# Optimization experiments

Measured on AMD Instinct MI355X. Metric: run time of the kernel, lower is better.

## Reference

```python
import jax, jax.numpy as jnp
import numpy as np

N = 100000      # nodes
E = 640000      # edges
VOCAB = 100     # Embedding(num_embeddings=100)
EMB = 10        # embed_dim
H = 128         # GCN hidden width


def gcn_conv(x, W, b, src, dst, n):
    """PyG GCNConv: linear (no bias) -> add self loops -> sym-normalized scatter-add -> +bias."""
    x = x @ W                                  # [n, out]
    loop = jnp.arange(n, dtype=src.dtype)
    src2 = jnp.concatenate([src, loop])        # [E+n]
    dst2 = jnp.concatenate([dst, loop])
    deg = jax.ops.segment_sum(jnp.ones_like(dst2, dtype=x.dtype), dst2, num_segments=n)
    dinv = jnp.where(deg > 0, jax.lax.rsqrt(deg), 0.0)
    norm = dinv[src2] * dinv[dst2]             # [E+n]
    out = jax.ops.segment_sum(x[src2] * norm[:, None], dst2, num_segments=n)
    return out + b


def setup_inputs() -> dict:
    key = jax.random.key(0)
    ks = jax.random.split(key, 9)
    x = jax.random.randint(ks[0], (N, 1), 0, VOCAB, dtype=jnp.int32)
    edge_index = jax.random.randint(ks[1], (2, E), 0, N, dtype=jnp.int32)
    batch = jnp.zeros((N,), dtype=jnp.int32)
    emb = jax.random.normal(ks[2], (VOCAB, EMB), dtype=jnp.float32)
    W1 = jax.random.normal(ks[3], (EMB, H), dtype=jnp.float32) * 0.1
    b1 = jnp.zeros((H,), dtype=jnp.float32)
    W2 = jax.random.normal(ks[4], (H, H), dtype=jnp.float32) * 0.1
    b2 = jnp.zeros((H,), dtype=jnp.float32)
    W3 = jax.random.normal(ks[5], (H, 1), dtype=jnp.float32) * 0.1
    b3 = jnp.zeros((1,), dtype=jnp.float32)
    return {"x": x, "edge_index": edge_index, "batch": batch,
            "emb": emb, "W1": W1, "b1": b1, "W2": W2, "b2": b2, "W3": W3, "b3": b3}


def reference(x, edge_index, batch, emb, W1, b1, W2, b2, W3, b3):
    # eval mode: dropout(p=0.5) is identity
    h = emb[x[:, 0]]                           # [N, EMB] embedding lookup + squeeze
    src, dst = edge_index[0], edge_index[1]
    n = h.shape[0]
    h = jax.nn.relu(gcn_conv(h, W1, b1, src, dst, n))   # [N, 128]
    h = jax.nn.relu(gcn_conv(h, W2, b2, src, dst, n))   # [N, 128]
    out = jax.nn.sigmoid((h @ W3 + b3).reshape(-1))      # [N]
    return out
```

## Files before the change

kernel.cpp:

```cpp
#include <hip/hip_runtime.h>
#include <math.h>

#define HDIM 128
#define EMBD 10
#define CAP  32
#define ZSTRIDE 136

typedef __attribute__((ext_vector_type(8))) short short8;
typedef __attribute__((ext_vector_type(8))) unsigned short ushort8;
typedef __attribute__((ext_vector_type(4))) float float4a;
typedef __attribute__((ext_vector_type(2))) float float2a;
typedef __attribute__((ext_vector_type(2))) unsigned uint2a;

__device__ inline ushort bf16_rne(float f) {
    unsigned u = __float_as_uint(f);
    unsigned r = (u + 0x7fffu + ((u >> 16) & 1u)) >> 16;
    return (ushort)r;
}
__device__ inline float bf16_to_f(ushort u) {
    return __uint_as_float(((unsigned)u) << 16);
}

__global__ void k_prep(const float* __restrict__ emb, const float* __restrict__ W1,
                       const float* __restrict__ W2, ushort* __restrict__ Tb,
                       ushort* __restrict__ W2t, int* __restrict__ cnt,
                       int N, int vocab) {
    int t = blockIdx.x * 256 + threadIdx.x;
    if (t < N) cnt[t] = 0;
    if (t < vocab * HDIM) {
        int c = t >> 7, f = t & 127;
        float s = 0.f;
#pragma unroll
        for (int k = 0; k < EMBD; ++k) s += emb[c * EMBD + k] * W1[k * HDIM + f];
        Tb[t] = bf16_rne(s);
    }
    if (t < HDIM * HDIM) {
        int n = t >> 7, k = t & 127;
        W2t[t] = bf16_rne(W2[k * HDIM + n]);
    }
}

__global__ void k_fill(const int* __restrict__ src, const int* __restrict__ dst,
                       int* __restrict__ cnt, int* __restrict__ slot, int E) {
    int e = blockIdx.x * blockDim.x + threadIdx.x;
    if (e >= E) return;
    int d = dst[e];
    int p = atomicAdd(&cnt[d], 1);
    if (p < CAP) slot[(size_t)d * CAP + p] = src[e];
}

__global__ void k_meta(const int* __restrict__ x, const int* __restrict__ cnt,
                       unsigned* __restrict__ meta, int N) {
    int v = blockIdx.x * 256 + threadIdx.x;
    if (v >= N) return;
    meta[v] = ((unsigned)x[v] << 16) | (unsigned)bf16_rne(rsqrtf((float)cnt[v] + 1.0f));
}

__global__ __launch_bounds__(512) void k_gather1(const int* __restrict__ slot,
                                                 const int* __restrict__ cnt,
                                                 const unsigned* __restrict__ meta,
                                                 const ushort* __restrict__ Tb,
                                                 const float* __restrict__ b1,
                                                 unsigned char* __restrict__ Ap,
                                                 int N, int vocab) {
    __shared__ ushort TbL[100 * HDIM];
    int n8 = (vocab * HDIM) >> 3;
    for (int i = threadIdx.x; i < n8; i += 512)
        ((ushort8*)TbL)[i] = ((const ushort8*)Tb)[i];
    __syncthreads();

    int tid = blockIdx.x * 512 + threadIdx.x;
    int v = tid >> 4, q = tid & 15;
    if (v >= N) return;
    int deg = cnt[v];
    int m = min(deg, CAP);
    float dv = rsqrtf((float)deg + 1.0f);
    int total = m + 1;
    const int* slotv = slot + (size_t)v * CAP;

    float acc[8] = {0.f, 0.f, 0.f, 0.f, 0.f, 0.f, 0.f, 0.f};
    for (int base = 0; base < total; base += 8) {
        int4 sa = *(const int4*)(slotv + base);
        int4 sb = *(const int4*)(slotv + base + 4);
        int sv[8] = {sa.x, sa.y, sa.z, sa.w, sb.x, sb.y, sb.z, sb.w};
        const unsigned* mp[8];
#pragma unroll
        for (int t = 0; t < 8; ++t) {
            int idx = base + t;
            mp[t] = meta + ((idx < m) ? sv[t] : v);
        }
        unsigned m0, m1, m2, m3, m4, m5, m6, m7;
        asm volatile(
            "global_load_dword %0, %8, off\n\t"
            "global_load_dword %1, %9, off\n\t"
            "global_load_dword %2, %10, off\n\t"
            "global_load_dword %3, %11, off\n\t"
            "global_load_dword %4, %12, off\n\t"
            "global_load_dword %5, %13, off\n\t"
            "global_load_dword %6, %14, off\n\t"
            "global_load_dword %7, %15, off\n\t"
            "s_waitcnt vmcnt(0)"
            : "=&v"(m0), "=&v"(m1), "=&v"(m2), "=&v"(m3),
              "=&v"(m4), "=&v"(m5), "=&v"(m6), "=&v"(m7)
            : "v"(mp[0]), "v"(mp[1]), "v"(mp[2]), "v"(mp[3]),
              "v"(mp[4]), "v"(mp[5]), "v"(mp[6]), "v"(mp[7]));
        unsigned mm[8] = {m0, m1, m2, m3, m4, m5, m6, m7};
#pragma unroll
        for (int t = 0; t < 8; ++t) {
            float wt = (base + t <= m) ? bf16_to_f((ushort)(mm[t] & 0xffffu)) : 0.f;
            ushort8 y = *(const ushort8*)&TbL[(mm[t] >> 16) * HDIM + q * 8];
#pragma unroll
            for (int k = 0; k < 8; ++k) acc[k] += wt * bf16_to_f(y[k]);
        }
    }
    float4 bb0 = *(const float4*)(b1 + q * 8);
    float4 bb1 = *(const float4*)(b1 + q * 8 + 4);
    float bb[8] = {bb0.x, bb0.y, bb0.z, bb0.w, bb1.x, bb1.y, bb1.z, bb1.w};
    float o[8];
#pragma unroll
    for (int k = 0; k < 8; ++k)
        o[k] = dv * fmaxf(dv * acc[k] + bb[k], 0.f);
    unsigned lo = __builtin_amdgcn_cvt_pk_fp8_f32(o[0], o[1], 0u, false);
    lo = __builtin_amdgcn_cvt_pk_fp8_f32(o[2], o[3], lo, true);
    unsigned hi = __builtin_amdgcn_cvt_pk_fp8_f32(o[4], o[5], 0u, false);
    hi = __builtin_amdgcn_cvt_pk_fp8_f32(o[6], o[7], hi, true);
    uint2 ow = make_uint2(lo, hi);
    *(uint2*)(Ap + (size_t)v * HDIM + q * 8) = ow;
}

__global__ __launch_bounds__(256, 8) void k_conv2(const int* __restrict__ slot,
                                                  const int* __restrict__ cnt,
                                                  const unsigned char* __restrict__ Ap,
                                                  const ushort* __restrict__ W2t,
                                                  const float* __restrict__ b2,
                                                  const float* __restrict__ W3,
                                                  const float* __restrict__ b3,
                                                  float* __restrict__ out, int N) {
    __shared__ ushort Z[16 * ZSTRIDE];
    __shared__ float pbuf[4][16];
    int tid = threadIdx.x;
    int g = tid >> 4, q = tid & 15;
    int v0 = blockIdx.x * 16;
    int v = min(v0 + g, N - 1);

    int deg = cnt[v];
    int m = min(deg, CAP);
    float dv = rsqrtf((float)deg + 1.0f);
    int total = m + 1;
    const int* slotv = slot + (size_t)v * CAP;
    const unsigned char* aq = Ap + q * 8;

    float acc[8] = {0.f, 0.f, 0.f, 0.f, 0.f, 0.f, 0.f, 0.f};
    for (int base = 0; base < total; base += 8) {
        int4 sa = *(const int4*)(slotv + base);
        int4 sb = *(const int4*)(slotv + base + 4);
        int sv[8] = {sa.x, sa.y, sa.z, sa.w, sb.x, sb.y, sb.z, sb.w};
        const unsigned char* pp[8];
#pragma unroll
        for (int t = 0; t < 8; ++t) {
            int idx = base + t;
            int s = (idx < m) ? sv[t] : v;
            pp[t] = aq + (size_t)s * HDIM;
        }
        uint2a r0, r1, r2, r3, r4, r5, r6, r7;
        asm volatile(
            "global_load_dwordx2 %0, %8, off\n\t"
            "global_load_dwordx2 %1, %9, off\n\t"
            "global_load_dwordx2 %2, %10, off\n\t"
            "global_load_dwordx2 %3, %11, off\n\t"
            "global_load_dwordx2 %4, %12, off\n\t"
            "global_load_dwordx2 %5, %13, off\n\t"
            "global_load_dwordx2 %6, %14, off\n\t"
            "global_load_dwordx2 %7, %15, off\n\t"
            "s_waitcnt vmcnt(0)"
            : "=&v"(r0), "=&v"(r1), "=&v"(r2), "=&v"(r3),
              "=&v"(r4), "=&v"(r5), "=&v"(r6), "=&v"(r7)
            : "v"(pp[0]), "v"(pp[1]), "v"(pp[2]), "v"(pp[3]),
              "v"(pp[4]), "v"(pp[5]), "v"(pp[6]), "v"(pp[7]));
        uint2a rr[8] = {r0, r1, r2, r3, r4, r5, r6, r7};
#pragma unroll
        for (int t = 0; t < 8; ++t) {
            float wt = (base + t <= m) ? 1.f : 0.f;
            float2a f01 = __builtin_amdgcn_cvt_pk_f32_fp8(rr[t][0], false);
            float2a f23 = __builtin_amdgcn_cvt_pk_f32_fp8(rr[t][0], true);
            float2a f45 = __builtin_amdgcn_cvt_pk_f32_fp8(rr[t][1], false);
            float2a f67 = __builtin_amdgcn_cvt_pk_f32_fp8(rr[t][1], true);
            acc[0] += wt * f01.x; acc[1] += wt * f01.y;
            acc[2] += wt * f23.x; acc[3] += wt * f23.y;
            acc[4] += wt * f45.x; acc[5] += wt * f45.y;
            acc[6] += wt * f67.x; acc[7] += wt * f67.y;
        }
    }
    ushort8 z;
#pragma unroll
    for (int k = 0; k < 8; ++k) z[k] = bf16_rne(dv * acc[k]);
    *(ushort8*)&Z[g * ZSTRIDE + q * 8] = z;
    __syncthreads();

    int lane = tid & 63, w = tid >> 6;
    int l15 = lane & 15, g4 = lane >> 4;
    short8 af[4];
#pragma unroll
    for (int kt = 0; kt < 4; ++kt)
        af[kt] = *(const short8*)&Z[l15 * ZSTRIDE + kt * 32 + g4 * 8];

    float pr[4] = {0.f, 0.f, 0.f, 0.f};
#pragma unroll
    for (int i = 0; i < 2; ++i) {
        int nt = w * 2 + i;
        int col = nt * 16 + l15;
        const ushort* bp = W2t + (size_t)col * HDIM + g4 * 8;
        float4a accD = {0.f, 0.f, 0.f, 0.f};
#pragma unroll
        for (int kt = 0; kt < 4; ++kt) {
            short8 bf = *(const short8*)(bp + kt * 32);
            accD = __builtin_amdgcn_mfma_f32_16x16x32_bf16(af[kt], bf, accD, 0, 0, 0);
        }
        float bc = b2[col], wc = W3[col];
#pragma unroll
        for (int r = 0; r < 4; ++r)
            pr[r] += fmaxf(accD[r] + bc, 0.f) * wc;
    }
#pragma unroll
    for (int off = 1; off < 16; off <<= 1) {
#pragma unroll
        for (int r = 0; r < 4; ++r) pr[r] += __shfl_xor(pr[r], off, 16);
    }
    if (l15 == 0) {
#pragma unroll
        for (int r = 0; r < 4; ++r) pbuf[w][g4 * 4 + r] = pr[r];
    }
    __syncthreads();
    if (tid < 16) {
        int row = tid;
        float s = pbuf[0][row] + pbuf[1][row] + pbuf[2][row] + pbuf[3][row];
        int vr = v0 + row;
        if (vr < N) out[vr] = 1.f / (1.f + expf(-(s + b3[0])));
    }
}

extern "C" void kernel_launch(void* const* d_in, const int* in_sizes, int n_in,
                              void* d_out, int out_size, void* d_ws, size_t ws_size,
                              hipStream_t stream) {
    const int*   x    = (const int*)d_in[0];
    const int*   ei   = (const int*)d_in[1];
    const float* emb  = (const float*)d_in[3];
    const float* W1   = (const float*)d_in[4];
    const float* b1   = (const float*)d_in[5];
    const float* W2   = (const float*)d_in[6];
    const float* b2   = (const float*)d_in[7];
    const float* W3   = (const float*)d_in[8];
    const float* b3   = (const float*)d_in[9];
    float*       out  = (float*)d_out;

    int N = in_sizes[0];
    int E = in_sizes[1] / 2;
    int vocab = in_sizes[3] / EMBD;
    const int* src = ei;
    const int* dst = ei + E;

    char* w = (char*)d_ws;
    ushort*        Tb   = (ushort*)w;         w += (size_t)vocab * HDIM * 2;
    unsigned char* Ap   = (unsigned char*)w;  w += (size_t)N * HDIM;
    ushort*        W2t  = (ushort*)w;         w += (size_t)HDIM * HDIM * 2;
    int*           cnt  = (int*)w;            w += (size_t)N * 4;
    unsigned*      meta = (unsigned*)w;       w += (size_t)N * 4;
    int*           slot = (int*)w;            w += (size_t)N * CAP * 4 + 64;

    int prep_elems = N;
    if (vocab * HDIM > prep_elems) prep_elems = vocab * HDIM;
    if (HDIM * HDIM > prep_elems) prep_elems = HDIM * HDIM;
    k_prep<<<(prep_elems + 255) / 256, 256, 0, stream>>>(emb, W1, W2, Tb, W2t, cnt, N, vocab);
    k_fill<<<(E + 255) / 256, 256, 0, stream>>>(src, dst, cnt, slot, E);
    k_meta<<<(N + 255) / 256, 256, 0, stream>>>(x, cnt, meta, N);

    int g1blocks = (int)(((long long)N * 16 + 511) / 512);
    k_gather1<<<g1blocks, 512, 0, stream>>>(slot, cnt, meta, Tb, b1, Ap, N, vocab);

    int cblocks = (N + 15) / 16;
    k_conv2<<<cblocks, 256, 0, stream>>>(slot, cnt, Ap, W2t, b2, W3, b3, out, N);
}
```

Measured before the change: 178.5 us.

## Process 32 nodes per block in conv2 with 16-byte fp8 gathers

Each conv2 block now handles 32 nodes instead of 16. Each thread owns 16 features and fetches them with dwordx4 loads instead of dwordx2, which halves the gather load instructions per edge and lets each block's W2 fragment loads feed twice as many rows in the MFMA stage. Each wave now computes 4 output column tiles for one 16-row block instead of 2 tiles. Register pressure rises (16 accumulators and wider load registers), and the launch bound occupancy hint drops from 8 to 6, which risks less latency hiding on the irregular gathers.

After: 174.8 us. -2.1%, faster.

```diff
diff --git a/kernel.cpp b/kernel.cpp
--- a/kernel.cpp
+++ b/kernel.cpp
@@ -11,6 +11,7 @@
 typedef __attribute__((ext_vector_type(4))) float float4a;
 typedef __attribute__((ext_vector_type(2))) float float2a;
 typedef __attribute__((ext_vector_type(2))) unsigned uint2a;
+typedef __attribute__((ext_vector_type(4))) unsigned uint4a;
 
 __device__ inline ushort bf16_rne(float f) {
     unsigned u = __float_as_uint(f);
@@ -128,7 +129,7 @@
     *(uint2*)(Ap + (size_t)v * HDIM + q * 8) = ow;
 }
 
-__global__ __launch_bounds__(256, 8) void k_conv2(const int* __restrict__ slot,
+__global__ __launch_bounds__(256, 6) void k_conv2(const int* __restrict__ slot,
                                                   const int* __restrict__ cnt,
                                                   const unsigned char* __restrict__ Ap,
                                                   const ushort* __restrict__ W2t,
@@ -136,11 +137,11 @@
                                                   const float* __restrict__ W3,
                                                   const float* __restrict__ b3,
                                                   float* __restrict__ out, int N) {
-    __shared__ ushort Z[16 * ZSTRIDE];
+    __shared__ ushort Z[32 * ZSTRIDE];
     __shared__ float pbuf[4][16];
     int tid = threadIdx.x;
-    int g = tid >> 4, q = tid & 15;
-    int v0 = blockIdx.x * 16;
+    int g = tid >> 3, q = tid & 7;
+    int v0 = blockIdx.x * 32;
     int v = min(v0 + g, N - 1);
 
     int deg = cnt[v];
@@ -148,9 +149,12 @@
     float dv = rsqrtf((float)deg + 1.0f);
     int total = m + 1;
     const int* slotv = slot + (size_t)v * CAP;
-    const unsigned char* aq = Ap + q * 8;
-
-    float acc[8] = {0.f, 0.f, 0.f, 0.f, 0.f, 0.f, 0.f, 0.f};
+    const unsigned char* aq = Ap + q * 16;
+
+    float acc[16];
+#pragma unroll
+    for (int k = 0; k < 16; ++k) acc[k] = 0.f;
+
     for (int base = 0; base < total; base += 8) {
         int4 sa = *(const int4*)(slotv + base);
         int4 sb = *(const int4*)(slotv + base + 4);
@@ -162,52 +166,58 @@
             int s = (idx < m) ? sv[t] : v;
             pp[t] = aq + (size_t)s * HDIM;
         }
-        uint2a r0, r1, r2, r3, r4, r5, r6, r7;
+        uint4a r0, r1, r2, r3, r4, r5, r6, r7;
         asm volatile(
-            "global_load_dwordx2 %0, %8, off\n\t"
-            "global_load_dwordx2 %1, %9, off\n\t"
-            "global_load_dwordx2 %2, %10, off\n\t"
-            "global_load_dwordx2 %3, %11, off\n\t"
-            "global_load_dwordx2 %4, %12, off\n\t"
-            "global_load_dwordx2 %5, %13, off\n\t"
-            "global_load_dwordx2 %6, %14, off\n\t"
-            "global_load_dwordx2 %7, %15, off\n\t"
+            "global_load_dwordx4 %0, %8, off\n\t"
+            "global_load_dwordx4 %1, %9, off\n\t"
+            "global_load_dwordx4 %2, %10, off\n\t"
+            "global_load_dwordx4 %3, %11, off\n\t"
+            "global_load_dwordx4 %4, %12, off\n\t"
+            "global_load_dwordx4 %5, %13, off\n\t"
+            "global_load_dwordx4 %6, %14, off\n\t"
+            "global_load_dwordx4 %7, %15, off\n\t"
             "s_waitcnt vmcnt(0)"
             : "=&v"(r0), "=&v"(r1), "=&v"(r2), "=&v"(r3),
               "=&v"(r4), "=&v"(r5), "=&v"(r6), "=&v"(r7)
             : "v"(pp[0]), "v"(pp[1]), "v"(pp[2]), "v"(pp[3]),
               "v"(pp[4]), "v"(pp[5]), "v"(pp[6]), "v"(pp[7]));
-        uint2a rr[8] = {r0, r1, r2, r3, r4, r5, r6, r7};
+        uint4a rr[8] = {r0, r1, r2, r3, r4, r5, r6, r7};
 #pragma unroll
         for (int t = 0; t < 8; ++t) {
             float wt = (base + t <= m) ? 1.f : 0.f;
-            float2a f01 = __builtin_amdgcn_cvt_pk_f32_fp8(rr[t][0], false);
-            float2a f23 = __builtin_amdgcn_cvt_pk_f32_fp8(rr[t][0], true);
-            float2a f45 = __builtin_amdgcn_cvt_pk_f32_fp8(rr[t][1], false);
-            float2a f67 = __builtin_amdgcn_cvt_pk_f32_fp8(rr[t][1], true);
-            acc[0] += wt * f01.x; acc[1] += wt * f01.y;
-            acc[2] += wt * f23.x; acc[3] += wt * f23.y;
-            acc[4] += wt * f45.x; acc[5] += wt * f45.y;
-            acc[6] += wt * f67.x; acc[7] += wt * f67.y;
-        }
-    }
-    ushort8 z;
-#pragma unroll
-    for (int k = 0; k < 8; ++k) z[k] = bf16_rne(dv * acc[k]);
-    *(ushort8*)&Z[g * ZSTRIDE + q * 8] = z;
+#pragma unroll
+            for (int d = 0; d < 4; ++d) {
+                float2a flo = __builtin_amdgcn_cvt_pk_f32_fp8(rr[t][d], false);
+                float2a fhi = __builtin_amdgcn_cvt_pk_f32_fp8(rr[t][d], true);
+                acc[d * 4 + 0] += wt * flo.x;
+                acc[d * 4 + 1] += wt * flo.y;
+                acc[d * 4 + 2] += wt * fhi.x;
+                acc[d * 4 + 3] += wt * fhi.y;
+            }
+        }
+    }
+    ushort8 z0, z1;
+#pragma unroll
+    for (int k = 0; k < 8; ++k) {
+        z0[k] = bf16_rne(dv * acc[k]);
+        z1[k] = bf16_rne(dv * acc[8 + k]);
+    }
+    *(ushort8*)&Z[g * ZSTRIDE + q * 16] = z0;
+    *(ushort8*)&Z[g * ZSTRIDE + q * 16 + 8] = z1;
     __syncthreads();
 
     int lane = tid & 63, w = tid >> 6;
     int l15 = lane & 15, g4 = lane >> 4;
+    int rb = w >> 1, ch = w & 1;
     short8 af[4];
 #pragma unroll
     for (int kt = 0; kt < 4; ++kt)
-        af[kt] = *(const short8*)&Z[l15 * ZSTRIDE + kt * 32 + g4 * 8];
+        af[kt] = *(const short8*)&Z[(rb * 16 + l15) * ZSTRIDE + kt * 32 + g4 * 8];
 
     float pr[4] = {0.f, 0.f, 0.f, 0.f};
 #pragma unroll
-    for (int i = 0; i < 2; ++i) {
-        int nt = w * 2 + i;
+    for (int i = 0; i < 4; ++i) {
+        int nt = ch * 4 + i;
         int col = nt * 16 + l15;
         const ushort* bp = W2t + (size_t)col * HDIM + g4 * 8;
         float4a accD = {0.f, 0.f, 0.f, 0.f};
@@ -231,9 +241,10 @@
         for (int r = 0; r < 4; ++r) pbuf[w][g4 * 4 + r] = pr[r];
     }
     __syncthreads();
-    if (tid < 16) {
+    if (tid < 32) {
         int row = tid;
-        float s = pbuf[0][row] + pbuf[1][row] + pbuf[2][row] + pbuf[3][row];
+        int rb2 = row >> 4, r15 = row & 15;
+        float s = pbuf[2 * rb2][r15] + pbuf[2 * rb2 + 1][r15];
         int vr = v0 + row;
         if (vr < N) out[vr] = 1.f / (1.f + expf(-(s + b3[0])));
     }
@@ -277,6 +288,6 @@
     int g1blocks = (int)(((long long)N * 16 + 511) / 512);
     k_gather1<<<g1blocks, 512, 0, stream>>>(slot, cnt, meta, Tb, b1, Ap, N, vocab);
 
-    int cblocks = (N + 15) / 16;
+    int cblocks = (N + 31) / 32;
     k_conv2<<<cblocks, 256, 0, stream>>>(slot, cnt, Ap, W2t, b2, W3, b3, out, N);
 }
```
